# Kernel tuning notes

Measured on AMD Instinct MI355X. Metric: run time of the kernel, lower is better.

## Reference

```python
import jax, jax.numpy as jnp
import numpy as np

# --- stochastic-computing constants (match FSUMGUCell defaults) ---
BW_W = 8                      # FSULinearPC weight bitstream bitwidth
BW_M = 4                      # FSUMul bitwidth (shift-register depth)
DEPTH = 10                    # FSUAdd accumulator depth
ACC_MAX = 2.0 ** (DEPTH - 2)  # +256
ACC_MIN = -ACC_MAX
NW = 2 ** BW_W
NM = 2 ** BW_M
# deterministic pseudo-random comparison sequences (stand-in for UnarySim Sobol RNG)
_RNG_W = jnp.asarray(np.random.RandomState(0).permutation(NW), dtype=jnp.float32)
_RNG_WI = jnp.asarray(np.random.RandomState(1).permutation(NW), dtype=jnp.float32)
_RNG_M = jnp.asarray(np.random.RandomState(2).permutation(NM), dtype=jnp.float32)


def _fsu_add(acc, s, offset, scale):
    # FSUAdd (bipolar): accumulate (parallel count - offset), clamp, emit bit when acc >= scale
    acc = jnp.clip(acc + s - offset, ACC_MIN, ACC_MAX)
    out = (acc >= scale).astype(jnp.float32)
    return acc - out * scale, out


def _linear_pc(x_aug, w_src, t):
    # FSULinearPC (bipolar): weight bits generated by rate coding (source > rng[t]),
    # XNOR with input bits, summed into a parallel count. x_aug: [B, F+1] (bias col of 1s).
    wb_p = (w_src > _RNG_W[t % NW]).astype(jnp.float32)   # [O, F+1]
    wb_i = (w_src > _RNG_WI[t % NW]).astype(jnp.float32)
    return x_aug @ wb_p.T + (1.0 - x_aug) @ (1.0 - wb_i).T


def _fsu_mul(state, in0, in1):
    # FSUMul non-static bipolar: estimate P(in1) with a BW_M-bit shift register,
    # regenerate a bit via rng comparison; XNOR-style pos/inv paths gated by in0,
    # with conditionally-advanced rng indices (enable-signal semantics).
    sr, idx_p, idx_i = state
    sr = jnp.concatenate([sr[1:], in1[None]], axis=0)      # shift in newest bit
    cnt = sr.sum(0) * (NM / BW_M)                          # scale count to rng range
    bit_p = (cnt > _RNG_M[idx_p % NM]).astype(jnp.float32)
    bit_i = (cnt > _RNG_M[idx_i % NM]).astype(jnp.float32)
    out = in0 * bit_p + (1.0 - in0) * (1.0 - bit_i)        # disjoint paths -> OR == +
    idx_p = idx_p + in0.astype(jnp.int32)
    idx_i = idx_i + (1 - in0.astype(jnp.int32))
    return (sr, idx_p, idx_i), out


def _w_src(w, b):
    # SourceGen bipolar: binary value in [-1,1] -> integer source in [0, 2^BW_W]
    aug = jnp.concatenate([w, b[:, None]], axis=1)
    return jnp.round((jnp.clip(aug, -1.0, 1.0) + 1.0) * 0.5 * NW)


def _forward(x_bits, hx0, weight_ih, bias_ih, weight_hh, bias_hh):
    T, B, I = x_bits.shape
    H = hx0.shape[1]
    src_ih = _w_src(weight_ih, bias_ih)   # [2H, I+1]
    src_hh = _w_src(weight_hh, bias_hh)   # [2H, H+1]
    ones_col = jnp.ones((B, 1), jnp.float32)
    acc0 = jnp.zeros((B, H), jnp.float32)
    sr0 = jnp.tile((jnp.arange(BW_M) % 2).astype(jnp.float32)[:, None, None], (1, B, H))
    mul0 = (sr0, jnp.zeros((B, H), jnp.int32), jnp.zeros((B, H), jnp.int32))
    off_fg = (I + H + 2 - 1) / 2.0        # entry=I+H+2, scaled=False -> scale=1

    def step(carry, xt):
        h, a1, a2, a3, a4, a5, a6, m1, m2, m3, t = carry
        gate_i = _linear_pc(jnp.concatenate([xt, ones_col], 1), src_ih, t)  # [B, 2H]
        gate_h = _linear_pc(jnp.concatenate([h, ones_col], 1), src_hh, t)
        i_f, i_n = gate_i[:, :H], gate_i[:, H:]
        h_f, h_n = gate_h[:, :H], gate_h[:, H:]
        a1, fg_in = _fsu_add(a1, i_f + h_f, off_fg, 1.0)
        a2, fg = _fsu_add(a2, fg_in + 1.0, 0.0, 2.0)          # scaled (x+1)/2 hardsigmoid
        a3, h_n_bit = _fsu_add(a3, h_n, H / 2.0, 1.0)          # entry=H+1
        m1, ng_prod = _fsu_mul(m1, fg, h_n_bit)
        a4, i_n_bit = _fsu_add(a4, i_n, I / 2.0, 1.0)          # entry=I+1
        a5, ng = _fsu_add(a5, i_n_bit + ng_prod, 0.5, 1.0)     # entry=2
        m2, fgi_prod = _fsu_mul(m2, 1.0 - fg, ng)
        m3, fg_prod = _fsu_mul(m3, fg, h)
        a6, hy = _fsu_add(a6, ng + fgi_prod + fg_prod, 1.0, 1.0)  # entry=3
        return (hy, a1, a2, a3, a4, a5, a6, m1, m2, m3, t + 1), hy

    carry0 = (hx0, acc0, acc0, acc0, acc0, acc0, acc0, mul0, mul0, mul0, jnp.int32(0))
    _, hy_stream = jax.lax.scan(step, carry0, x_bits)
    return hy_stream  # [T, B, H] unary bitstream of hidden state


def setup_inputs():
    key = jax.random.key(0)
    ks = jax.random.split(key, 6)
    T, B, I, H = 64, 128, 1024, 1024
    x_bits = jax.random.bernoulli(ks[0], 0.5, (T, B, I)).astype(jnp.float32)
    hx0 = jax.random.bernoulli(ks[1], 0.5, (B, H)).astype(jnp.float32)
    weight_ih = jax.random.uniform(ks[2], (2 * H, I), jnp.float32, -1.0, 1.0)
    bias_ih = jax.random.uniform(ks[3], (2 * H,), jnp.float32, -1.0, 1.0)
    weight_hh = jax.random.uniform(ks[4], (2 * H, H), jnp.float32, -1.0, 1.0)
    bias_hh = jax.random.uniform(ks[5], (2 * H,), jnp.float32, -1.0, 1.0)
    return {"x_bits": x_bits, "hx0": hx0, "weight_ih": weight_ih, "bias_ih": bias_ih,
            "weight_hh": weight_hh, "bias_hh": bias_hh}


def reference(x_bits, hx0, weight_ih, bias_ih, weight_hh, bias_hh):
    return _forward(x_bits, hx0, weight_ih, bias_ih, weight_hh, bias_hh)
```

## Files before the change

kernel.cpp:

```cpp
#include <hip/hip_runtime.h>


#define NBLK 256
#define NTHR 1024

#define WS_BAR_SUB   0u
#define WS_BAR_MST   1024u
#define WS_BAR_FLG   2048u
#define WS_RNGW   8192u
#define WS_RNGWI  9216u
#define WS_RNGM   10240u
#define WS_SRCB   12288u
#define WS_SRCW   20480u
#define WS_XP     8409088u
#define WS_HW     9457664u
#define WS_DT     9523200u
#define WS_MASKS  10571776u

struct SRng {
  unsigned mt[3][624];
  unsigned yb[3][624];
  unsigned draws[3][1248];
  int perm[3][256];
};
struct SC {
  unsigned short rows[16][1028];
  int rngw[64];
  int rngwi[64];
};
struct SL {
  unsigned long long mask2[2][64*34];
  unsigned xb[32*34];
  unsigned short hrow16[32*68];
  int rngm[16];
};
union SU { SRng r; SC c; SL l; };

__device__ __forceinline__ unsigned mt_temper(unsigned y){
  y ^= y >> 11;
  y ^= (y << 7)  & 0x9d2c5680u;
  y ^= (y << 15) & 0xefc60000u;
  y ^= y >> 18;
  return y;
}

__device__ void mt_regen_serial(unsigned* mt){
  for (int i = 0; i < 624; i++){
    unsigned y = (mt[i] & 0x80000000u) | (mt[(i+1)%624] & 0x7fffffffu);
    mt[i] = mt[(i+397)%624] ^ (y >> 1) ^ ((y & 1u) ? 0x9908b0dfu : 0u);
  }
}

__device__ void rng_gen(SU* sm, int* rngw, int* rngwi, int* rngm){
  const int tid = threadIdx.x;
  const int wv = tid >> 6, lane = tid & 63;
  const bool act = (wv < 3);
  if (act && lane == 0){
    unsigned* mt = sm->r.mt[wv];
    mt[0] = (unsigned)wv;
    for (int i = 1; i < 624; i++)
      mt[i] = 1812433253u * (mt[i-1] ^ (mt[i-1] >> 30)) + (unsigned)i;
  }
  __syncthreads();
  for (int r = 0; r < 2; r++){
    if (act){
      unsigned* mt = sm->r.mt[wv]; unsigned* yb = sm->r.yb[wv];
      for (int i = lane; i < 623; i += 64)
        yb[i] = (mt[i] & 0x80000000u) | (mt[i+1] & 0x7fffffffu);
    }
    __syncthreads();
    if (act){
      unsigned* mt = sm->r.mt[wv]; unsigned* yb = sm->r.yb[wv];
      for (int i = lane; i < 227; i += 64){
        unsigned y = yb[i];
        mt[i] = mt[i+397] ^ (y >> 1) ^ ((y & 1u) ? 0x9908b0dfu : 0u);
      }
    }
    __syncthreads();
    if (act){
      unsigned* mt = sm->r.mt[wv]; unsigned* yb = sm->r.yb[wv];
      for (int i = 227 + lane; i < 454; i += 64){
        unsigned y = yb[i];
        mt[i] = mt[i-227] ^ (y >> 1) ^ ((y & 1u) ? 0x9908b0dfu : 0u);
      }
    }
    __syncthreads();
    if (act){
      unsigned* mt = sm->r.mt[wv]; unsigned* yb = sm->r.yb[wv];
      for (int i = 454 + lane; i < 624; i += 64){
        unsigned y = (i < 623) ? yb[i]
                   : ((mt[623] & 0x80000000u) | (mt[0] & 0x7fffffffu));
        mt[i] = mt[i-227] ^ (y >> 1) ^ ((y & 1u) ? 0x9908b0dfu : 0u);
      }
    }
    __syncthreads();
    if (act){
      unsigned* mt = sm->r.mt[wv];
      for (int i = lane; i < 624; i += 64)
        sm->r.draws[wv][r*624 + i] = mt_temper(mt[i]);
    }
    __syncthreads();
  }
  if (act && lane == 0){
    const int n = (wv == 2) ? 16 : 256;
    int* perm = sm->r.perm[wv];
    for (int i = 0; i < n; i++) perm[i] = i;
    int dp = 0, spos = 624;
    unsigned* mt = sm->r.mt[wv];
    for (int i = n - 1; i > 0; i--){
      unsigned mask = (unsigned)i;
      mask |= mask >> 1; mask |= mask >> 2; mask |= mask >> 4;
      mask |= mask >> 8; mask |= mask >> 16;
      unsigned v;
      do {
        unsigned d;
        if (dp < 1248) d = sm->r.draws[wv][dp++];
        else {
          if (spos >= 624){ mt_regen_serial(mt); spos = 0; }
          d = mt_temper(mt[spos++]);
        }
        v = d & mask;
      } while (v > (unsigned)i);
      int tmp = perm[i]; perm[i] = perm[v]; perm[v] = tmp;
    }
    int* dst = (wv == 0) ? rngw : (wv == 1) ? rngwi : rngm;
    for (int i = 0; i < n; i++) dst[i] = perm[i];
  }
}

__device__ __forceinline__ void gbar_full(unsigned char* ws, unsigned ep){
  __syncthreads();
  if (threadIdx.x == 0){
    __threadfence();
    unsigned* sub = (unsigned*)(ws + WS_BAR_SUB + (blockIdx.x & 7)*128);
    unsigned old = atomicAdd(sub, 1u);
    if (old == ep*32u - 1u){
      unsigned* mst = (unsigned*)(ws + WS_BAR_MST);
      unsigned mo = atomicAdd(mst, 1u);
      if (mo == ep*8u - 1u){
        for (int i = 0; i < 8; i++)
          __hip_atomic_store((unsigned*)(ws + WS_BAR_FLG + i*128), ep,
                             __ATOMIC_RELAXED, __HIP_MEMORY_SCOPE_AGENT);
      }
    }
    const unsigned* fl = (const unsigned*)(ws + WS_BAR_FLG + (blockIdx.x & 7)*128);
    while (__hip_atomic_load(fl, __ATOMIC_RELAXED, __HIP_MEMORY_SCOPE_AGENT) < ep)
      __builtin_amdgcn_s_sleep(8);
  }
  __syncthreads();
  __threadfence();
}

__device__ __forceinline__ int clampi(int v){
  v = v < -512 ? -512 : v;
  v = v >  512 ?  512 : v;
  return v;
}

__device__ __forceinline__ unsigned bfi(unsigned x, unsigned p, unsigned n){
  return (x & p) | (~x & n);
}

__global__ void __launch_bounds__(NTHR)
fsu_kernel(const float* __restrict__ x, const float* __restrict__ hx0,
           const float* __restrict__ wih, const float* __restrict__ bih,
           const float* __restrict__ whh, const float* __restrict__ bhh,
           float* __restrict__ out, unsigned char* __restrict__ ws)
{
  __shared__ SU sm;
  const int tid = threadIdx.x;
  const int bid = blockIdx.x;

  int* rngw  = (int*)(ws + WS_RNGW);
  int* rngwi = (int*)(ws + WS_RNGWI);
  int* rngm  = (int*)(ws + WS_RNGM);
  unsigned short* srcb = (unsigned short*)(ws + WS_SRCB);
  unsigned short* srcw = (unsigned short*)(ws + WS_SRCW);
  unsigned* xp   = (unsigned*)(ws + WS_XP);
  unsigned long long* hw = (unsigned long long*)(ws + WS_HW);
  int* Dt = (int*)(ws + WS_DT);
  unsigned long long* masks = (unsigned long long*)(ws + WS_MASKS);

  if (bid == 0){
    rng_gen(&sm, rngw, rngwi, rngm);
  } else {
    const int gtid = (bid - 1)*NTHR + tid;
    const int lane = tid & 63;
    const int gw = gtid >> 6;
    const int nw = (NBLK-1)*(NTHR/64);
    const int nthr = (NBLK-1)*NTHR;
    for (int ch = gw; ch < 131072; ch += nw){
      float v = x[(size_t)ch*64 + lane];
      unsigned long long bal = __ballot(v != 0.0f);
      if ((lane & 31) == 0) xp[ch*2 + (lane >> 5)] = (unsigned)(bal >> lane);
    }
    for (int idx = gtid; idx < 4096; idx += nthr){
      int bg2 = idx >> 10, jt2 = (idx >> 4) & 63, rp2 = idx & 15;
      int r0 = bg2*32 + 2*rp2;
      unsigned v = 0;
      for (int j = 0; j < 16; j++){
        v |= (hx0[(size_t)r0*1024 + jt2*16 + j] != 0.0f) ? (1u<<j) : 0u;
        v |= (hx0[(size_t)(r0+1)*1024 + jt2*16 + j] != 0.0f) ? (1u<<(16+j)) : 0u;
      }
      hw[idx] = (unsigned long long)v;
    }
    for (int idx = gtid; idx < 4096*1024; idx += nthr){
      int c = idx >> 10, k = idx & 1023;
      float wv2 = (c < 2048) ? wih[(size_t)c*1024 + k] : whh[(size_t)(c - 2048)*1024 + k];
      float cl = fminf(fmaxf(wv2, -1.0f), 1.0f);
      srcw[idx] = (unsigned short)(int)rintf((cl + 1.0f)*0.5f*256.0f);
    }
    for (int c = gtid; c < 4096; c += nthr){
      float bv = (c < 2048) ? bih[c] : bhh[c - 2048];
      float cl = fminf(fmaxf(bv, -1.0f), 1.0f);
      srcb[c] = (unsigned short)(int)rintf((cl + 1.0f)*0.5f*256.0f);
    }
  }
  gbar_full(ws, 1u);

  {
    const int c0 = bid * 16;
    const unsigned* srcw32 = (const unsigned*)srcw;
    for (int q = tid; q < 16*512; q += NTHR){
      int r = q >> 9, w = q & 511;
      ((unsigned*)&sm.c.rows[r][0])[w] = srcw32[(size_t)(c0 + r)*512 + w];
    }
    if (tid < 64) sm.c.rngw[tid] = rngw[tid];
    if (tid >= 64 && tid < 128) sm.c.rngwi[tid - 64] = rngwi[tid - 64];
    __syncthreads();
    for (int row = tid; row < 1024; row += NTHR){
      int t = row >> 4, lc = row & 15, col = c0 + lc;
      int rp = sm.c.rngw[t], ri = sm.c.rngwi[t];
      int hi = rp > ri ? rp : ri;
      int lo1 = (rp < ri ? rp : ri) + 1;
      bool rihi = (ri >= rp);
      const unsigned* srow = (const unsigned*)&sm.c.rows[lc][0];
      unsigned long long* gdst = masks + ((size_t)t*4096 + col)*32;
      int cnti = 0, cntn = 0;
      for (int w = 0; w < 32; w++){
        unsigned pos = 0, neg = 0;
        #pragma unroll
        for (int i2 = 15; i2 >= 0; i2--){
          unsigned v2 = srow[w*16 + i2];
          int vH = (int)(v2 >> 16);
          int vL = (int)(v2 & 0xFFFFu);
          pos = (pos << 1) | ((unsigned)(hi - vH) >> 31);
          neg = (neg << 1) | ((unsigned)(vH - lo1) >> 31);
          pos = (pos << 1) | ((unsigned)(hi - vL) >> 31);
          neg = (neg << 1) | ((unsigned)(vL - lo1) >> 31);
        }
        gdst[w] = (unsigned long long)pos | ((unsigned long long)neg << 32);
        cnti += rihi ? __popc(pos) : (32 - __popc(neg));
        cntn += __popc(neg);
      }
      Dt[t*4096 + col] = 1024 - cnti - cntn + (((int)srcb[col] > rp) ? 1 : 0);
    }
  }
  gbar_full(ws, 2u);

  const int jt = bid & 63, bg = bid >> 6;
  const int j0 = jt * 16, b0 = bg * 32;
  const int kh  = (tid >> 5) & 1;
  const int o   = ((tid >> 6) << 5) + (tid & 31);
  const int b_l = o >> 4, j_l = o & 15;
  const int bglob = b0 + b_l;
  const int w2lo = kh << 3;

  int hcur = (hx0[(size_t)bglob*1024 + j0 + j_l] != 0.0f) ? 1 : 0;
  int A1=0,A2=0,A3=0,A4=0,A5=0,A6=0;
  unsigned sr1=10u, sr2=10u, sr3=10u;
  int i1p=0,i1i=0,i2p=0,i2i=0,i3p=0,i3i=0;

  if (tid < 16) sm.l.rngm[tid] = rngm[tid];

  const unsigned* msrc = (const unsigned*)masks;
  int cur = 0;
  int xgf, xgn, dhf, dhn;
  unsigned mreg[4], xreg;
  int dreg[4];

  {
    unsigned* mbuf = (unsigned*)sm.l.mask2[0];
    #pragma unroll
    for (int i = 0; i < 4; i++){
      int q = tid + i*NTHR;
      int r = q >> 6, qq = q & 63;
      int c = (r >> 4)*1024 + j0 + (r & 15);
      mbuf[r*68 + qq] = msrc[((size_t)0*4096 + c)*64 + qq];
    }
    {
      int bb = tid >> 5, w = tid & 31;
      sm.l.xb[bb*34 + w] = xp[((size_t)0*128 + b0 + bb)*32 + w];
    }
    {
      unsigned long long v = __hip_atomic_load(&hw[(size_t)bg*1024 + tid],
                                               __ATOMIC_RELAXED,
                                               __HIP_MEMORY_SCOPE_AGENT);
      int jt_ = tid >> 4, rp_ = tid & 15;
      unsigned data = (unsigned)v;
      sm.l.hrow16[(2*rp_)*68 + jt_]   = (unsigned short)(data & 0xFFFFu);
      sm.l.hrow16[(2*rp_+1)*68 + jt_] = (unsigned short)(data >> 16);
    }
    #pragma unroll
    for (int g = 0; g < 4; g++) dreg[g] = Dt[0*4096 + g*1024 + j0 + j_l];
    __syncthreads();
    int s0=0, s1=0;
    const uint2* xrow = (const uint2*)&sm.l.xb[b_l*34];
    const ulonglong2* m0p = (const ulonglong2*)&sm.l.mask2[0][(0  + j_l)*34];
    const ulonglong2* m1p = (const ulonglong2*)&sm.l.mask2[0][(16 + j_l)*34];
    #pragma unroll
    for (int w2i = 0; w2i < 8; w2i++){
      int w2 = w2lo + w2i;
      uint2 xv = xrow[w2];
      ulonglong2 a = m0p[w2];
      s0 += __popc(bfi(xv.x, (unsigned)a.x, (unsigned)(a.x >> 32)));
      s0 += __popc(bfi(xv.y, (unsigned)a.y, (unsigned)(a.y >> 32)));
      ulonglong2 b = m1p[w2];
      s1 += __popc(bfi(xv.x, (unsigned)b.x, (unsigned)(b.x >> 32)));
      s1 += __popc(bfi(xv.y, (unsigned)b.y, (unsigned)(b.y >> 32)));
    }
    s0 += __shfl_xor(s0, 32);
    s1 += __shfl_xor(s1, 32);
    xgf = dreg[0] + s0;
    xgn = dreg[1] + s1;
    dhf = dreg[2]; dhn = dreg[3];
    #pragma unroll
    for (int i = 0; i < 4; i++){
      int q = tid + i*NTHR;
      int r = q >> 6, qq = q & 63;
      int c = (r >> 4)*1024 + j0 + (r & 15);
      mreg[i] = msrc[((size_t)1*4096 + c)*64 + qq];
    }
    {
      int bb = tid >> 5, w = tid & 31;
      xreg = xp[((size_t)1*128 + b0 + bb)*32 + w];
    }
    #pragma unroll
    for (int g = 0; g < 4; g++) dreg[g] = Dt[1*4096 + g*1024 + j0 + j_l];
  }

  for (int t = 0; t < 64; t++){
    const int par = t & 1;

    int s2=0, s3=0;
    {
      const uint2* hrow = (const uint2*)&sm.l.hrow16[b_l*68];
      const ulonglong2* m2p = (const ulonglong2*)&sm.l.mask2[cur][(32 + j_l)*34];
      const ulonglong2* m3p = (const ulonglong2*)&sm.l.mask2[cur][(48 + j_l)*34];
      #pragma unroll
      for (int w2i = 0; w2i < 8; w2i++){
        int w2 = w2lo + w2i;
        uint2 hv = hrow[w2];
        ulonglong2 c2 = m2p[w2];
        s2 += __popc(bfi(hv.x, (unsigned)c2.x, (unsigned)(c2.x >> 32)));
        s2 += __popc(bfi(hv.y, (unsigned)c2.y, (unsigned)(c2.y >> 32)));
        ulonglong2 d = m3p[w2];
        s3 += __popc(bfi(hv.x, (unsigned)d.x, (unsigned)(d.x >> 32)));
        s3 += __popc(bfi(hv.y, (unsigned)d.y, (unsigned)(d.y >> 32)));
      }
    }
    s2 += __shfl_xor(s2, 32);
    s3 += __shfl_xor(s3, 32);
    const int g_hf = dhf + s2;
    const int g_hn = dhn + s3;

    int s1v = xgf + g_hf;
    A1 = clampi(A1 + 2*s1v - 2049);
    int fg_in = (A1 >= 2); A1 -= fg_in << 1;
    A2 = clampi(A2 + ((fg_in + 1) << 1));
    int fg = (A2 >= 4); A2 -= fg << 2;
    A3 = clampi(A3 + (g_hn << 1) - 1024);
    int hnb = (A3 >= 2); A3 -= hnb << 1;

    sr1 = ((sr1 >> 1) | ((unsigned)hnb << 3)) & 0xFu;
    int ng_prod;
    {
      int cv = __popc(sr1) << 2;
      int bp = cv > sm.l.rngm[i1p & 15];
      int bi = cv > sm.l.rngm[i1i & 15];
      ng_prod = fg ? bp : (1 - bi);
      i1p += fg; i1i += 1 - fg;
    }
    A4 = clampi(A4 + (xgn << 1) - 1024);
    int inb = (A4 >= 2); A4 -= inb << 1;
    A5 = clampi(A5 + ((inb + ng_prod) << 1) - 1);
    int ng = (A5 >= 2); A5 -= ng << 1;

    sr2 = ((sr2 >> 1) | ((unsigned)ng << 3)) & 0xFu;
    int fgi;
    {
      int cv = __popc(sr2) << 2;
      int bp = cv > sm.l.rngm[i2p & 15];
      int bi = cv > sm.l.rngm[i2i & 15];
      fgi = (1 - fg) ? bp : (1 - bi);
      i2p += 1 - fg; i2i += fg;
    }
    sr3 = ((sr3 >> 1) | ((unsigned)hcur << 3)) & 0xFu;
    int fgp;
    {
      int cv = __popc(sr3) << 2;
      int bp = cv > sm.l.rngm[i3p & 15];
      int bi = cv > sm.l.rngm[i3i & 15];
      fgp = fg ? bp : (1 - bi);
      i3p += fg; i3i += 1 - fg;
    }
    A6 = clampi(A6 + ((ng + fgi + fgp) << 1) - 2);
    int hy = (A6 >= 2); A6 -= hy << 1;
    hcur = hy;

    if (t < 63){
      unsigned long long bal = __ballot(hy);
      if ((tid & 63) == 0){
        unsigned data = (unsigned)bal;
        unsigned long long val = (unsigned long long)data
                               | ((unsigned long long)(unsigned)(t + 1) << 32);
        __hip_atomic_store(
            &hw[(((size_t)((par ^ 1)*4 + bg))*64 + jt)*16 + (tid >> 6)], val,
            __ATOMIC_RELAXED, __HIP_MEMORY_SCOPE_AGENT);
      }
    }
    if (kh == 0)
      out[(size_t)t*131072 + (size_t)bglob*1024 + j0 + j_l] = (float)hy;
    if (t == 63) break;

    {
      unsigned* mbuf = (unsigned*)sm.l.mask2[cur ^ 1];
      #pragma unroll
      for (int i = 0; i < 4; i++){
        int q = tid + i*NTHR;
        int r = q >> 6, qq = q & 63;
        mbuf[r*68 + qq] = mreg[i];
      }
      int bb = tid >> 5, w = tid & 31;
      sm.l.xb[bb*34 + w] = xreg;
    }
    __syncthreads();

    {
      int s0=0, s1b=0;
      const uint2* xrow = (const uint2*)&sm.l.xb[b_l*34];
      const ulonglong2* m0p = (const ulonglong2*)&sm.l.mask2[cur ^ 1][(0  + j_l)*34];
      const ulonglong2* m1p = (const ulonglong2*)&sm.l.mask2[cur ^ 1][(16 + j_l)*34];
      #pragma unroll
      for (int w2i = 0; w2i < 8; w2i++){
        int w2 = w2lo + w2i;
        uint2 xv = xrow[w2];
        ulonglong2 a = m0p[w2];
        s0 += __popc(bfi(xv.x, (unsigned)a.x, (unsigned)(a.x >> 32)));
        s0 += __popc(bfi(xv.y, (unsigned)a.y, (unsigned)(a.y >> 32)));
        ulonglong2 b = m1p[w2];
        s1b += __popc(bfi(xv.x, (unsigned)b.x, (unsigned)(b.x >> 32)));
        s1b += __popc(bfi(xv.y, (unsigned)b.y, (unsigned)(b.y >> 32)));
      }
      s0 += __shfl_xor(s0, 32);
      s1b += __shfl_xor(s1b, 32);
      xgf = dreg[0] + s0;
      xgn = dreg[1] + s1b;
      dhf = dreg[2]; dhn = dreg[3];
    }

    if (t < 62){
      #pragma unroll
      for (int i = 0; i < 4; i++){
        int q = tid + i*NTHR;
        int r = q >> 6, qq = q & 63;
        int c = (r >> 4)*1024 + j0 + (r & 15);
        mreg[i] = msrc[((size_t)(t+2)*4096 + c)*64 + qq];
      }
      {
        int bb = tid >> 5, w = tid & 31;
        xreg = xp[((size_t)(t+2)*128 + b0 + bb)*32 + w];
      }
      #pragma unroll
      for (int g = 0; g < 4; g++)
        dreg[g] = Dt[(t+2)*4096 + g*1024 + j0 + j_l];
    }

    {
      const unsigned ep = (unsigned)(t + 1);
      const unsigned long long* slot =
          &hw[((size_t)((par ^ 1)*4 + bg))*1024 + tid];
      unsigned long long v = __hip_atomic_load(slot, __ATOMIC_RELAXED,
                                               __HIP_MEMORY_SCOPE_AGENT);
      while ((unsigned)(v >> 32) < ep){
        __builtin_amdgcn_s_sleep(1);
        v = __hip_atomic_load(slot, __ATOMIC_RELAXED,
                              __HIP_MEMORY_SCOPE_AGENT);
      }
      int jt_ = tid >> 4, rp_ = tid & 15;
      unsigned data = (unsigned)v;
      sm.l.hrow16[(2*rp_)*68 + jt_]   = (unsigned short)(data & 0xFFFFu);
      sm.l.hrow16[(2*rp_+1)*68 + jt_] = (unsigned short)(data >> 16);
    }
    __syncthreads();
    cur ^= 1;
  }
}

extern "C" void kernel_launch(void* const* d_in, const int* in_sizes, int n_in,
                              void* d_out, int out_size, void* d_ws, size_t ws_size,
                              hipStream_t stream)
{
  (void)in_sizes; (void)n_in; (void)out_size; (void)ws_size;
  const float* x   = (const float*)d_in[0];
  const float* hx0 = (const float*)d_in[1];
  const float* wih = (const float*)d_in[2];
  const float* bih = (const float*)d_in[3];
  const float* whh = (const float*)d_in[4];
  const float* bhh = (const float*)d_in[5];
  float* out = (float*)d_out;
  unsigned char* ws = (unsigned char*)d_ws;

  hipMemsetAsync(d_ws, 0, 4096, stream);
  hipMemsetAsync(ws + WS_HW, 0, 65536, stream);

  void* args[] = { (void*)&x, (void*)&hx0, (void*)&wih, (void*)&bih,
                   (void*)&whh, (void*)&bhh, (void*)&out, (void*)&ws };
  hipLaunchCooperativeKernel(reinterpret_cast<void*>(fsu_kernel),
                             dim3(NBLK), dim3(NTHR), args, 0, stream);
}
```

Before: 481.2 us.

## Precompute input-gate popcounts for all timesteps before recurrent loop

Adds a pre-phase in which every block computes the x-path gate counts (input masks against packed x bits) for one timestep and batch quarter, packs the two gates into 16-bit halves, and writes them to a workspace pool. That pool reuses the mask region, so a grid barrier is placed before the writes. The recurrent loop then only streams and popcounts the hidden-weight masks, loads one precomputed word per step, and double-buffers hrow16 so one __syncthreads per step can be dropped. This takes the x-path work off the serial critical path, at the cost of two extra grid barriers and extra global traffic; the spin sleep is also lengthened.

After: 1.416 ms. 194% more time.

```diff
diff --git a/kernel.cpp b/kernel.cpp
--- a/kernel.cpp
+++ b/kernel.cpp
@@ -28,13 +28,15 @@
   int rngw[64];
   int rngwi[64];
 };
+struct SD {
+  unsigned xst[32*32];
+};
 struct SL {
-  unsigned long long mask2[2][64*34];
-  unsigned xb[32*34];
-  unsigned short hrow16[32*68];
+  unsigned long long hmask[2][32*34];
+  unsigned short hrow16[2][32*68];
   int rngm[16];
 };
-union SU { SRng r; SC c; SL l; };
+union SU { SRng r; SC c; SD d; SL l; };
 
 __device__ __forceinline__ unsigned mt_temper(unsigned y){
   y ^= y >> 11;
@@ -180,6 +182,7 @@
   unsigned long long* hw = (unsigned long long*)(ws + WS_HW);
   int* Dt = (int*)(ws + WS_DT);
   unsigned long long* masks = (unsigned long long*)(ws + WS_MASKS);
+  unsigned* xgpool = (unsigned*)(ws + WS_MASKS);
 
   if (bid == 0){
     rng_gen(&sm, rngw, rngwi, rngm);
@@ -258,6 +261,49 @@
   }
   gbar_full(ws, 2u);
 
+  {
+    const int tD = bid >> 2, bq = bid & 3;
+    {
+      int b_l = tid >> 5, w = tid & 31;
+      sm.d.xst[b_l*32 + w] = xp[((size_t)tD*128 + bq*32 + b_l)*32 + w];
+    }
+    __syncthreads();
+    const int jcol = tid;
+    int dA = Dt[tD*4096 + jcol] + 2048;
+    int dB = Dt[tD*4096 + 1024 + jcol] + 2048;
+    unsigned acc[32];
+    #pragma unroll
+    for (int b = 0; b < 32; b++) acc[b] = (unsigned)dA | ((unsigned)dB << 16);
+    const uint4* mA = (const uint4*)(masks + ((size_t)tD*4096 + jcol)*32);
+    const uint4* mB = (const uint4*)(masks + ((size_t)tD*4096 + 1024 + jcol)*32);
+    for (int c = 0; c < 4; c++){
+      uint4 a0 = mA[c*4+0], a1 = mA[c*4+1], a2 = mA[c*4+2], a3 = mA[c*4+3];
+      uint4 g0 = mB[c*4+0], g1 = mB[c*4+1], g2 = mB[c*4+2], g3 = mB[c*4+3];
+      #pragma unroll
+      for (int b = 0; b < 32; b++){
+        const uint4* xv = (const uint4*)&sm.d.xst[b*32 + c*8];
+        uint4 x0 = xv[0], x1 = xv[1];
+        unsigned sA =
+            __popc(bfi(x0.x, a0.x, a0.y)) + __popc(bfi(x0.y, a0.z, a0.w)) +
+            __popc(bfi(x0.z, a1.x, a1.y)) + __popc(bfi(x0.w, a1.z, a1.w)) +
+            __popc(bfi(x1.x, a2.x, a2.y)) + __popc(bfi(x1.y, a2.z, a2.w)) +
+            __popc(bfi(x1.z, a3.x, a3.y)) + __popc(bfi(x1.w, a3.z, a3.w));
+        unsigned sB =
+            __popc(bfi(x0.x, g0.x, g0.y)) + __popc(bfi(x0.y, g0.z, g0.w)) +
+            __popc(bfi(x0.z, g1.x, g1.y)) + __popc(bfi(x0.w, g1.z, g1.w)) +
+            __popc(bfi(x1.x, g2.x, g2.y)) + __popc(bfi(x1.y, g2.z, g2.w)) +
+            __popc(bfi(x1.z, g3.x, g3.y)) + __popc(bfi(x1.w, g3.z, g3.w));
+        acc[b] += sA + (sB << 16);
+      }
+    }
+    gbar_full(ws, 3u);
+    unsigned* xgst = xgpool + (size_t)tD*262144;
+    #pragma unroll
+    for (int b = 0; b < 32; b++)
+      xgst[(size_t)(bq*32 + b)*1024 + jcol] = acc[b];
+  }
+  gbar_full(ws, 4u);
+
   const int jt = bid & 63, bg = bid >> 6;
   const int j0 = jt * 16, b0 = bg * 32;
   const int kh  = (tid >> 5) & 1;
@@ -265,8 +311,9 @@
   const int b_l = o >> 4, j_l = o & 15;
   const int bglob = b0 + b_l;
   const int w2lo = kh << 3;
-
-  int hcur = (hx0[(size_t)bglob*1024 + j0 + j_l] != 0.0f) ? 1 : 0;
+  const int jcol = j0 + j_l;
+
+  int hcur = (hx0[(size_t)bglob*1024 + jcol] != 0.0f) ? 1 : 0;
   int A1=0,A2=0,A3=0,A4=0,A5=0,A6=0;
   unsigned sr1=10u, sr2=10u, sr3=10u;
   int i1p=0,i1i=0,i2p=0,i2i=0,i3p=0,i3i=0;
@@ -275,22 +322,18 @@
 
   const unsigned* msrc = (const unsigned*)masks;
   int cur = 0;
-  int xgf, xgn, dhf, dhn;
-  unsigned mreg[4], xreg;
-  int dreg[4];
+  unsigned mreg[2];
+  unsigned xg_cur, xg_nxt;
+  int dhf, dhn, dh_nf, dh_nn;
 
   {
-    unsigned* mbuf = (unsigned*)sm.l.mask2[0];
+    unsigned* mbuf = (unsigned*)sm.l.hmask[0];
     #pragma unroll
-    for (int i = 0; i < 4; i++){
+    for (int i = 0; i < 2; i++){
       int q = tid + i*NTHR;
       int r = q >> 6, qq = q & 63;
-      int c = (r >> 4)*1024 + j0 + (r & 15);
+      int c = 2048 + (r >> 4)*1024 + j0 + (r & 15);
       mbuf[r*68 + qq] = msrc[((size_t)0*4096 + c)*64 + qq];
-    }
-    {
-      int bb = tid >> 5, w = tid & 31;
-      sm.l.xb[bb*34 + w] = xp[((size_t)0*128 + b0 + bb)*32 + w];
     }
     {
       unsigned long long v = __hip_atomic_load(&hw[(size_t)bg*1024 + tid],
@@ -298,45 +341,23 @@
                                                __HIP_MEMORY_SCOPE_AGENT);
       int jt_ = tid >> 4, rp_ = tid & 15;
       unsigned data = (unsigned)v;
-      sm.l.hrow16[(2*rp_)*68 + jt_]   = (unsigned short)(data & 0xFFFFu);
-      sm.l.hrow16[(2*rp_+1)*68 + jt_] = (unsigned short)(data >> 16);
-    }
+      sm.l.hrow16[0][(2*rp_)*68 + jt_]   = (unsigned short)(data & 0xFFFFu);
+      sm.l.hrow16[0][(2*rp_+1)*68 + jt_] = (unsigned short)(data >> 16);
+    }
+    xg_cur = xgpool[(size_t)0*262144 + (size_t)bglob*1024 + jcol];
+    xg_nxt = xgpool[(size_t)1*262144 + (size_t)bglob*1024 + jcol];
+    dhf   = Dt[0*4096 + 2048 + jcol];
+    dhn   = Dt[0*4096 + 3072 + jcol];
+    dh_nf = Dt[1*4096 + 2048 + jcol];
+    dh_nn = Dt[1*4096 + 3072 + jcol];
     #pragma unroll
-    for (int g = 0; g < 4; g++) dreg[g] = Dt[0*4096 + g*1024 + j0 + j_l];
-    __syncthreads();
-    int s0=0, s1=0;
-    const uint2* xrow = (const uint2*)&sm.l.xb[b_l*34];
-    const ulonglong2* m0p = (const ulonglong2*)&sm.l.mask2[0][(0  + j_l)*34];
-    const ulonglong2* m1p = (const ulonglong2*)&sm.l.mask2[0][(16 + j_l)*34];
-    #pragma unroll
-    for (int w2i = 0; w2i < 8; w2i++){
-      int w2 = w2lo + w2i;
-      uint2 xv = xrow[w2];
-      ulonglong2 a = m0p[w2];
-      s0 += __popc(bfi(xv.x, (unsigned)a.x, (unsigned)(a.x >> 32)));
-      s0 += __popc(bfi(xv.y, (unsigned)a.y, (unsigned)(a.y >> 32)));
-      ulonglong2 b = m1p[w2];
-      s1 += __popc(bfi(xv.x, (unsigned)b.x, (unsigned)(b.x >> 32)));
-      s1 += __popc(bfi(xv.y, (unsigned)b.y, (unsigned)(b.y >> 32)));
-    }
-    s0 += __shfl_xor(s0, 32);
-    s1 += __shfl_xor(s1, 32);
-    xgf = dreg[0] + s0;
-    xgn = dreg[1] + s1;
-    dhf = dreg[2]; dhn = dreg[3];
-    #pragma unroll
-    for (int i = 0; i < 4; i++){
+    for (int i = 0; i < 2; i++){
       int q = tid + i*NTHR;
       int r = q >> 6, qq = q & 63;
-      int c = (r >> 4)*1024 + j0 + (r & 15);
+      int c = 2048 + (r >> 4)*1024 + j0 + (r & 15);
       mreg[i] = msrc[((size_t)1*4096 + c)*64 + qq];
     }
-    {
-      int bb = tid >> 5, w = tid & 31;
-      xreg = xp[((size_t)1*128 + b0 + bb)*32 + w];
-    }
-    #pragma unroll
-    for (int g = 0; g < 4; g++) dreg[g] = Dt[1*4096 + g*1024 + j0 + j_l];
+    __syncthreads();
   }
 
   for (int t = 0; t < 64; t++){
@@ -344,9 +365,9 @@
 
     int s2=0, s3=0;
     {
-      const uint2* hrow = (const uint2*)&sm.l.hrow16[b_l*68];
-      const ulonglong2* m2p = (const ulonglong2*)&sm.l.mask2[cur][(32 + j_l)*34];
-      const ulonglong2* m3p = (const ulonglong2*)&sm.l.mask2[cur][(48 + j_l)*34];
+      const uint2* hrow = (const uint2*)&sm.l.hrow16[cur][b_l*68];
+      const ulonglong2* m2p = (const ulonglong2*)&sm.l.hmask[cur][(0  + j_l)*34];
+      const ulonglong2* m3p = (const ulonglong2*)&sm.l.hmask[cur][(16 + j_l)*34];
       #pragma unroll
       for (int w2i = 0; w2i < 8; w2i++){
         int w2 = w2lo + w2i;
@@ -363,6 +384,8 @@
     s3 += __shfl_xor(s3, 32);
     const int g_hf = dhf + s2;
     const int g_hn = dhn + s3;
+    const int xgf = (int)(xg_cur & 0xFFFFu) - 2048;
+    const int xgn = (int)(xg_cur >> 16) - 2048;
 
     int s1v = xgf + g_hf;
     A1 = clampi(A1 + 2*s1v - 2049);
@@ -420,60 +443,30 @@
       }
     }
     if (kh == 0)
-      out[(size_t)t*131072 + (size_t)bglob*1024 + j0 + j_l] = (float)hy;
+      out[(size_t)t*131072 + (size_t)bglob*1024 + jcol] = (float)hy;
     if (t == 63) break;
 
     {
-      unsigned* mbuf = (unsigned*)sm.l.mask2[cur ^ 1];
+      unsigned* mbuf = (unsigned*)sm.l.hmask[cur ^ 1];
       #pragma unroll
-      for (int i = 0; i < 4; i++){
+      for (int i = 0; i < 2; i++){
+        int q = tid + i*NTHR;
+        mbuf[(q >> 6)*68 + (q & 63)] = mreg[i];
+      }
+    }
+
+    xg_cur = xg_nxt; dhf = dh_nf; dhn = dh_nn;
+    if (t < 62){
+      #pragma unroll
+      for (int i = 0; i < 2; i++){
         int q = tid + i*NTHR;
         int r = q >> 6, qq = q & 63;
-        mbuf[r*68 + qq] = mreg[i];
-      }
-      int bb = tid >> 5, w = tid & 31;
-      sm.l.xb[bb*34 + w] = xreg;
-    }
-    __syncthreads();
-
-    {
-      int s0=0, s1b=0;
-      const uint2* xrow = (const uint2*)&sm.l.xb[b_l*34];
-      const ulonglong2* m0p = (const ulonglong2*)&sm.l.mask2[cur ^ 1][(0  + j_l)*34];
-      const ulonglong2* m1p = (const ulonglong2*)&sm.l.mask2[cur ^ 1][(16 + j_l)*34];
-      #pragma unroll
-      for (int w2i = 0; w2i < 8; w2i++){
-        int w2 = w2lo + w2i;
-        uint2 xv = xrow[w2];
-        ulonglong2 a = m0p[w2];
-        s0 += __popc(bfi(xv.x, (unsigned)a.x, (unsigned)(a.x >> 32)));
-        s0 += __popc(bfi(xv.y, (unsigned)a.y, (unsigned)(a.y >> 32)));
-        ulonglong2 b = m1p[w2];
-        s1b += __popc(bfi(xv.x, (unsigned)b.x, (unsigned)(b.x >> 32)));
-        s1b += __popc(bfi(xv.y, (unsigned)b.y, (unsigned)(b.y >> 32)));
-      }
-      s0 += __shfl_xor(s0, 32);
-      s1b += __shfl_xor(s1b, 32);
-      xgf = dreg[0] + s0;
-      xgn = dreg[1] + s1b;
-      dhf = dreg[2]; dhn = dreg[3];
-    }
-
-    if (t < 62){
-      #pragma unroll
-      for (int i = 0; i < 4; i++){
-        int q = tid + i*NTHR;
-        int r = q >> 6, qq = q & 63;
-        int c = (r >> 4)*1024 + j0 + (r & 15);
+        int c = 2048 + (r >> 4)*1024 + j0 + (r & 15);
         mreg[i] = msrc[((size_t)(t+2)*4096 + c)*64 + qq];
       }
-      {
-        int bb = tid >> 5, w = tid & 31;
-        xreg = xp[((size_t)(t+2)*128 + b0 + bb)*32 + w];
-      }
-      #pragma unroll
-      for (int g = 0; g < 4; g++)
-        dreg[g] = Dt[(t+2)*4096 + g*1024 + j0 + j_l];
+      xg_nxt = xgpool[(size_t)(t+2)*262144 + (size_t)bglob*1024 + jcol];
+      dh_nf = Dt[(t+2)*4096 + 2048 + jcol];
+      dh_nn = Dt[(t+2)*4096 + 3072 + jcol];
     }
 
     {
@@ -483,14 +476,14 @@
       unsigned long long v = __hip_atomic_load(slot, __ATOMIC_RELAXED,
                                                __HIP_MEMORY_SCOPE_AGENT);
       while ((unsigned)(v >> 32) < ep){
-        __builtin_amdgcn_s_sleep(1);
+        __builtin_amdgcn_s_sleep(2);
         v = __hip_atomic_load(slot, __ATOMIC_RELAXED,
                               __HIP_MEMORY_SCOPE_AGENT);
       }
       int jt_ = tid >> 4, rp_ = tid & 15;
       unsigned data = (unsigned)v;
-      sm.l.hrow16[(2*rp_)*68 + jt_]   = (unsigned short)(data & 0xFFFFu);
-      sm.l.hrow16[(2*rp_+1)*68 + jt_] = (unsigned short)(data >> 16);
+      sm.l.hrow16[cur ^ 1][(2*rp_)*68 + jt_]   = (unsigned short)(data & 0xFFFFu);
+      sm.l.hrow16[cur ^ 1][(2*rp_+1)*68 + jt_] = (unsigned short)(data >> 16);
     }
     __syncthreads();
     cur ^= 1;
```
